# Kernel tuning notes

Hardware: AMD Instinct MI355X
Metric: run time of the kernel (lower is better)

Reference implementation:

```python
import jax, jax.numpy as jnp
import numpy as np

EMB = 1024
HEADS = 16
HEAD = EMB // HEADS
B, S = 4, 1024


def setup_inputs() -> dict:
    key = jax.random.key(0)
    ks = jax.random.split(key, 8)
    glorot = lambda k, shp: jax.random.normal(k, shp, jnp.float32) * np.sqrt(2.0 / (shp[-2] + shp[-1]))
    return {
        "inputs_for_keys": jax.random.normal(ks[0], (B, S, EMB), jnp.float32),
        "inputs_for_values": jax.random.normal(ks[1], (B, S, EMB), jnp.float32),
        "inputs_for_queries": jax.random.normal(ks[2], (B, S, EMB), jnp.float32),
        "Wk": glorot(ks[3], (HEADS, EMB, HEAD)),
        "Wv": glorot(ks[4], (HEADS, EMB, HEAD)),
        "Wq": glorot(ks[5], (HEADS, EMB, HEAD)),
        "Wo": glorot(ks[6], (EMB, EMB)),
        "bo": jnp.zeros((EMB,), jnp.float32),
    }


def reference(inputs_for_keys, inputs_for_values, inputs_for_queries, Wk, Wv, Wq, Wo, bo):
    # Batched equivalent of the per-head loop: project all heads at once.
    K = jnp.einsum("bse,hed->bhsd", inputs_for_keys, Wk)
    V = jnp.einsum("bse,hed->bhsd", inputs_for_values, Wv)
    Q = jnp.einsum("bse,hed->bhsd", inputs_for_queries, Wq)
    s_keys = K.shape[2]
    s_q = Q.shape[2]
    # causal mask: -inf strictly above diagonal (original: np.triu(ones*-inf, k=1))
    mask = jnp.where(jnp.triu(jnp.ones((s_q, s_keys), bool), k=1), -jnp.inf, 0.0).astype(jnp.float32)
    logits = jnp.einsum("bhqd,bhkd->bhqk", Q, K)
    # FAITHFUL quirk: original divides (logits + mask) by sqrt(window_size_keys)
    scores = jax.nn.softmax((logits + mask) / np.sqrt(s_keys), axis=-1)
    ctx = jnp.einsum("bhqk,bhkd->bhqd", scores, V)  # [B,H,Sq,Dh]
    # concat heads along last dim (head order matches loop order)
    concat = ctx.transpose(0, 2, 1, 3).reshape(ctx.shape[0], s_q, -1)  # [B,Sq,E]
    return jax.nn.relu(concat @ Wo + bo)
```

## Files before the change

### kernel.cpp

```cpp
#include <hip/hip_runtime.h>
#include <hip/hip_bf16.h>

typedef unsigned short u16;
typedef unsigned int   u32;
typedef __attribute__((ext_vector_type(4))) float f32x4;
typedef __attribute__((ext_vector_type(8))) short bf16x8;
typedef __attribute__((ext_vector_type(4))) short bf16x4;

#define EMB   1024
#define SEQ   1024
#define HEADS 16
#define DH    64
#define BATCH 4
#define BH    64
#define BS    4096
#define LDP   72
#define NEG_BIG (-1.0e30f)

__device__ __forceinline__ float b2f(u16 u){ return __uint_as_float(((u32)u) << 16); }
__device__ __forceinline__ u16 f2b(float f){
    u32 u = __float_as_uint(f);
    u32 r = u + 0x7fffu + ((u >> 16) & 1u);
    return (u16)(r >> 16);
}
__device__ __forceinline__ void zero4(f32x4& v){ v[0]=0.f; v[1]=0.f; v[2]=0.f; v[3]=0.f; }
__device__ __forceinline__ ushort4 pk4(float a, float b, float c, float d){
    ushort4 p; p.x = f2b(a); p.y = f2b(b); p.z = f2b(c); p.w = f2b(d); return p;
}

__device__ __forceinline__ void gld_lds16(const void* g, void* l){
    __builtin_amdgcn_global_load_lds(
        (const __attribute__((address_space(1))) u32*)g,
        (__attribute__((address_space(3))) u32*)l, 16, 0, 0);
}

__device__ __forceinline__ u16* tptr(u16* base, int row, int col ){
    const int phys = ((col >> 3) ^ (row & 7));
    return base + row * 64 + (phys << 3);
}
__device__ __forceinline__ const u16* tptrc(const u16* base, int row, int col ){
    const int phys = ((col >> 3) ^ (row & 7));
    return base + row * 64 + (phys << 3);
}
__device__ __forceinline__ const u16* tptr8c(const u16* base, int row, int col ){
    const int chunk = ((col >> 3) ^ (row & 7));
    return base + row * 64 + (chunk << 3) + (col & 7);
}

__device__ __forceinline__ void dot2_f32(const float* __restrict__ x,
                                         const float* __restrict__ w, const int ws,
                                         float& a0, float& a1)
{
    float s0 = 0.f, s1 = 0.f;
    for (int e = 0; e < EMB; e += 4) {
        const float4 xv = *(const float4*)(x + e);
        const float2 w0 = *(const float2*)(w + (size_t)(e + 0) * ws);
        const float2 w1 = *(const float2*)(w + (size_t)(e + 1) * ws);
        const float2 w2 = *(const float2*)(w + (size_t)(e + 2) * ws);
        const float2 w3 = *(const float2*)(w + (size_t)(e + 3) * ws);
        s0 += xv.x * w0.x; s1 += xv.x * w0.y;
        s0 += xv.y * w1.x; s1 += xv.y * w1.y;
        s0 += xv.z * w2.x; s1 += xv.z * w2.y;
        s0 += xv.w * w3.x; s1 += xv.w * w3.y;
    }
    a0 = s0; a1 = s1;
}


__global__ __launch_bounds__(256) void convert_x(
    const float* __restrict__ Xk, const float* __restrict__ Xv, const float* __restrict__ Xq,
    u16* __restrict__ XB)
{
    const int which = blockIdx.y;
    const float* __restrict__ src = (which == 0) ? Xk : (which == 1) ? Xv : Xq;
    const size_t off = (size_t)blockIdx.x * 1024 + threadIdx.x * 4;
    const float4 v = *(const float4*)(src + off);
    *(ushort4*)(XB + (size_t)which * 4194304 + off) = pk4(v.x, v.y, v.z, v.w);
}

__global__ __launch_bounds__(256) void transpose_w(
    const float* __restrict__ Wk, const float* __restrict__ Wv, const float* __restrict__ Wq,
    const float* __restrict__ Wo, u16* __restrict__ WT, u16* __restrict__ WoT)
{
    __shared__ u16 T[64][LDP];
    const int which = blockIdx.y;
    const int bx = blockIdx.x, t = threadIdx.x;

    if (which < 3) {
        const float* __restrict__ W = (which == 0) ? Wk : (which == 1) ? Wv : Wq;
        const int h = bx >> 4, e0 = (bx & 15) * 64;
        #pragma unroll
        for (int i = 0; i < 16; ++i) {
            const int idx = i * 256 + t;
            const int e = idx >> 6, d = idx & 63;
            T[d][e] = f2b(W[(size_t)h * (EMB * DH) + (size_t)(e0 + e) * DH + d]);
        }
        __syncthreads();
        u16* dstb = WT + (size_t)which * (EMB * EMB / 16) * 16;
        #pragma unroll
        for (int i = 0; i < 2; ++i) {
            const int idx = i * 256 + t;
            const int d = idx >> 3, e8 = (idx & 7) * 8;
            *(bf16x8*)(dstb + (size_t)(h * 64 + d) * EMB + e0 + e8) = *(const bf16x8*)&T[d][e8];
        }
    } else {
        const int j0 = (bx >> 4) * 64, e0 = (bx & 15) * 64;
        #pragma unroll
        for (int i = 0; i < 16; ++i) {
            const int idx = i * 256 + t;
            const int e = idx >> 6, d = idx & 63;
            T[d][e] = f2b(Wo[(size_t)(e0 + e) * EMB + j0 + d]);
        }
        __syncthreads();
        #pragma unroll
        for (int i = 0; i < 2; ++i) {
            const int idx = i * 256 + t;
            const int d = idx >> 3, e8 = (idx & 7) * 8;
            *(bf16x8*)(WoT + (size_t)(j0 + d) * EMB + e0 + e8) = *(const bf16x8*)&T[d][e8];
        }
    }
}

template<int MODE>
__global__ __launch_bounds__(256) void gemm128(
    const u16* __restrict__ XB, const u16* __restrict__ WT,
    u16* __restrict__ Qw, u16* __restrict__ Kw, u16* __restrict__ Vt,
    const float* __restrict__ bo, float* __restrict__ OUT)
{
    __shared__ u16 As[128 * 64];
    __shared__ u16 Bs[128 * 64];

    const int t = threadIdx.x;
    const int wave = t >> 6, lane = t & 63;
    const int quad = lane >> 4, l16 = lane & 15;
    const int wrow = wave >> 1, wcol = wave & 1;
    const int m0 = blockIdx.x * 128;
    const int n0 = blockIdx.y * 128;
    const int which = blockIdx.z;

    const u16* __restrict__ Ag = (MODE == 0) ? XB + (size_t)which * 4194304 : XB;
    const u16* __restrict__ Bg = (MODE == 0) ? WT + (size_t)which * 1048576 : WT;

    f32x4 acc[4][4];
    #pragma unroll
    for (int mi = 0; mi < 4; ++mi)
        #pragma unroll
        for (int ni = 0; ni < 4; ++ni) zero4(acc[mi][ni]);

    for (int k0 = 0; k0 < EMB; k0 += 64) {
        #pragma unroll
        for (int j = 0; j < 4; ++j) {
            const int cg = wave * 4 + j;
            const int c  = cg * 64 + lane;
            const int row = c >> 3;
            const int col = ((c ^ row) & 7) << 3;
            gld_lds16(Ag + (size_t)(m0 + row) * EMB + k0 + col, As + cg * 512);
            gld_lds16(Bg + (size_t)(n0 + row) * EMB + k0 + col, Bs + cg * 512);
        }
        __syncthreads();

        #pragma unroll
        for (int kb = 0; kb < 2; ++kb) {
            bf16x8 af[4], bf[4];
            #pragma unroll
            for (int mi = 0; mi < 4; ++mi)
                af[mi] = *(const bf16x8*)tptr(As, wrow * 64 + mi * 16 + l16, kb * 32 + quad * 8);
            #pragma unroll
            for (int ni = 0; ni < 4; ++ni)
                bf[ni] = *(const bf16x8*)tptr(Bs, wcol * 64 + ni * 16 + l16, kb * 32 + quad * 8);
            #pragma unroll
            for (int mi = 0; mi < 4; ++mi)
                #pragma unroll
                for (int ni = 0; ni < 4; ++ni)
                    acc[mi][ni] = __builtin_amdgcn_mfma_f32_16x16x32_bf16(af[mi], bf[ni], acc[mi][ni], 0, 0, 0);
        }
        __syncthreads();
    }

    #pragma unroll
    for (int mi = 0; mi < 4; ++mi) {
        const int r = m0 + wrow * 64 + mi * 16 + quad * 4;
        #pragma unroll
        for (int ni = 0; ni < 4; ++ni) {
            const int j = n0 + wcol * 64 + ni * 16 + l16;
            if (MODE == 1) {
                const float bias = bo[j];
                #pragma unroll
                for (int reg = 0; reg < 4; ++reg) {
                    float v = acc[mi][ni][reg] + bias;
                    if (v < 0.f) v = 0.f;
                    OUT[(size_t)(r + reg) * EMB + j] = v;
                }
            } else {
                const int h = j >> 6, d = j & 63;
                const int b = r >> 10, s = r & (SEQ - 1);
                const int bh = b * HEADS + h;
                if (which == 1) {
                    *(ushort4*)(Vt + ((size_t)bh * DH + d) * SEQ + s) =
                        pk4(acc[mi][ni][0], acc[mi][ni][1], acc[mi][ni][2], acc[mi][ni][3]);
                } else {
                    u16* dst = (which == 0) ? Kw : Qw;
                    const float qsc = (which == 2) ? 0.03125f : 1.0f;
                    #pragma unroll
                    for (int reg = 0; reg < 4; ++reg)
                        dst[((size_t)bh * SEQ + s + reg) * DH + d] = f2b(acc[mi][ni][reg] * qsc);
                }
            }
        }
    }
}

__global__ __launch_bounds__(256) void attn_flash2(
    const u16* __restrict__ Qg, const u16* __restrict__ Kg, const u16* __restrict__ Vg,
    u16* __restrict__ CTXb)
{
    __shared__ u16 Ks[2][64 * 64];
    __shared__ u16 Vs[2][64 * 64];

    const int t = threadIdx.x;
    const int wave = t >> 6, lane = t & 63;
    const int quad = lane >> 4, l16 = lane & 15;
    const int bh = blockIdx.y;
    const int qt = (blockIdx.x + (blockIdx.y >> 2)) & 15;
    const int b = bh >> 4, h = bh & (HEADS - 1);
    const int q0 = qt * 64;

    const u16* __restrict__ Kbase = Kg + (size_t)bh * SEQ * DH;
    const u16* __restrict__ Vbase = Vg + (size_t)bh * DH * SEQ;

    bf16x8 qf[2];
    {
        const u16* qrow = Qg + ((size_t)bh * SEQ + q0 + wave * 16 + l16) * DH;
        qf[0] = *(const bf16x8*)(qrow + quad * 8);
        qf[1] = *(const bf16x8*)(qrow + 32 + quad * 8);
    }

    #pragma unroll
    for (int i = 0; i < 2; ++i) {
        const int c = i * 256 + t;
        const int row = c >> 3, col8 = (c & 7) * 8;
        const bf16x8 kv = *(const bf16x8*)(Kbase + (size_t)row * DH + col8);
        const bf16x8 vv = *(const bf16x8*)(Vbase + (size_t)row * SEQ + col8);
        *(bf16x8*)tptr(&Ks[0][0], row, col8) = kv;
        *(bf16x8*)tptr(&Vs[0][0], row, col8) = vv;
    }

    float m = NEG_BIG, l = 0.f;
    f32x4 oacc[4];
    #pragma unroll
    for (int nd = 0; nd < 4; ++nd) zero4(oacc[nd]);

    __syncthreads();

    const int qin = wave * 16 + l16;
    int cur = 0;
    for (int c = 0; c <= qt; ++c) {
        const int kn = ((c < qt) ? c + 1 : qt) * 64;
        bf16x8 kpre[2], vpre[2];
        #pragma unroll
        for (int i = 0; i < 2; ++i) {
            const int cc = i * 256 + t;
            const int row = cc >> 3, col8 = (cc & 7) * 8;
            kpre[i] = *(const bf16x8*)(Kbase + (size_t)(kn + row) * DH + col8);
            vpre[i] = *(const bf16x8*)(Vbase + (size_t)row * SEQ + kn + col8);
        }

        const u16* Kc = &Ks[cur][0];
        const u16* Vc = &Vs[cur][0];

        f32x4 sacc[4];
        #pragma unroll
        for (int ni = 0; ni < 4; ++ni) zero4(sacc[ni]);
        __builtin_amdgcn_s_setprio(1);
        #pragma unroll
        for (int kb = 0; kb < 2; ++kb) {
            #pragma unroll
            for (int ni = 0; ni < 4; ++ni) {
                const bf16x8 kf = *(const bf16x8*)tptrc(Kc, ni * 16 + l16, kb * 32 + quad * 8);
                sacc[ni] = __builtin_amdgcn_mfma_f32_16x16x32_bf16(kf, qf[kb], sacc[ni], 0, 0, 0);
            }
        }
        __builtin_amdgcn_s_setprio(0);

        const bool diag = (c == qt);
        float mx = m;
        #pragma unroll
        for (int ni = 0; ni < 4; ++ni) {
            #pragma unroll
            for (int reg = 0; reg < 4; ++reg) {
                float s = sacc[ni][reg];
                if (diag && (ni * 16 + quad * 4 + reg > qin)) s = NEG_BIG;
                sacc[ni][reg] = s;
                mx = fmaxf(mx, s);
            }
        }
        mx = fmaxf(mx, __shfl_xor(mx, 16));
        mx = fmaxf(mx, __shfl_xor(mx, 32));
        const float alpha = __expf(m - mx);
        m = mx;
        float rs = 0.f;
        bf16x4 pa[4];
        #pragma unroll
        for (int ni = 0; ni < 4; ++ni) {
            const float p0 = __expf(sacc[ni][0] - mx);
            const float p1 = __expf(sacc[ni][1] - mx);
            const float p2 = __expf(sacc[ni][2] - mx);
            const float p3 = __expf(sacc[ni][3] - mx);
            rs += (p0 + p1) + (p2 + p3);
            bf16x4 pk;
            pk[0] = (short)f2b(p0); pk[1] = (short)f2b(p1);
            pk[2] = (short)f2b(p2); pk[3] = (short)f2b(p3);
            pa[ni] = pk;
        }
        rs += __shfl_xor(rs, 16);
        rs += __shfl_xor(rs, 32);
        l = l * alpha + rs;

        #pragma unroll
        for (int reg = 0; reg < 4; ++reg) {
            const float ar = __shfl(alpha, quad * 4 + reg);
            #pragma unroll
            for (int nd = 0; nd < 4; ++nd) oacc[nd][reg] *= ar;
        }

        __builtin_amdgcn_s_setprio(1);
        #pragma unroll
        for (int ks = 0; ks < 4; ++ks) {
            #pragma unroll
            for (int nd = 0; nd < 4; ++nd) {
                const bf16x4 vf = *(const bf16x4*)tptr8c(Vc, nd * 16 + l16, ks * 16 + quad * 4);
                oacc[nd] = __builtin_amdgcn_mfma_f32_16x16x16bf16_1k(pa[ks], vf, oacc[nd], 0, 0, 0);
            }
        }
        __builtin_amdgcn_s_setprio(0);

        const int nxt = cur ^ 1;
        #pragma unroll
        for (int i = 0; i < 2; ++i) {
            const int cc = i * 256 + t;
            const int row = cc >> 3, col8 = (cc & 7) * 8;
            *(bf16x8*)tptr(&Ks[nxt][0], row, col8) = kpre[i];
            *(bf16x8*)tptr(&Vs[nxt][0], row, col8) = vpre[i];
        }
        __syncthreads();
        cur = nxt;
    }

    #pragma unroll
    for (int reg = 0; reg < 4; ++reg) {
        const float il = 1.f / __shfl(l, quad * 4 + reg);
        const int q = q0 + wave * 16 + quad * 4 + reg;
        #pragma unroll
        for (int nd = 0; nd < 4; ++nd) {
            const int d = nd * 16 + l16;
            CTXb[(size_t)(b * SEQ + q) * EMB + h * DH + d] = f2b(oacc[nd][reg] * il);
        }
    }
}


__global__ __launch_bounds__(256) void qkv_proj_mfma(
    const float* __restrict__ Xk, const float* __restrict__ Xv, const float* __restrict__ Xq,
    const float* __restrict__ Wk, const float* __restrict__ Wv, const float* __restrict__ Wq,
    u16* __restrict__ Kw, u16* __restrict__ Vw, u16* __restrict__ Qw)
{
    __shared__ u16 As[128][LDP];
    __shared__ u16 Bs[64][LDP];

    const int which = blockIdx.z;
    const float* __restrict__ X = (which == 0) ? Xk : (which == 1) ? Xv : Xq;
    const float* __restrict__ W = (which == 0) ? Wk : (which == 1) ? Wv : Wq;

    const int h    = blockIdx.y;
    const int m0   = blockIdx.x * 128;
    const int t    = threadIdx.x;
    const int wave = t >> 6, lane = t & 63;
    const int quad = lane >> 4, l16 = lane & 15;

    f32x4 acc[2][4];
    #pragma unroll
    for (int mi = 0; mi < 2; ++mi)
        #pragma unroll
        for (int ni = 0; ni < 4; ++ni) zero4(acc[mi][ni]);

    const size_t wbase = (size_t)h * EMB * DH;
    for (int k0 = 0; k0 < EMB; k0 += 64) {
        #pragma unroll
        for (int i = 0; i < 8; ++i) {
            const int idx = i * 256 + t;
            const int r = idx >> 4, c4 = (idx & 15) * 4;
            const float4 v = *(const float4*)(X + (size_t)(m0 + r) * EMB + k0 + c4);
            *(ushort4*)&As[r][c4] = pk4(v.x, v.y, v.z, v.w);
        }
        #pragma unroll
        for (int i = 0; i < 4; ++i) {
            const int d  = t & 63;
            const int e0 = (t >> 6) * 4 + i * 16;
            const float v0 = W[wbase + (size_t)(k0 + e0 + 0) * DH + d];
            const float v1 = W[wbase + (size_t)(k0 + e0 + 1) * DH + d];
            const float v2 = W[wbase + (size_t)(k0 + e0 + 2) * DH + d];
            const float v3 = W[wbase + (size_t)(k0 + e0 + 3) * DH + d];
            *(ushort4*)&Bs[d][e0] = pk4(v0, v1, v2, v3);
        }
        __syncthreads();

        #pragma unroll
        for (int kb = 0; kb < 2; ++kb) {
            bf16x8 bfr[4];
            #pragma unroll
            for (int ni = 0; ni < 4; ++ni)
                bfr[ni] = *(const bf16x8*)&Bs[ni * 16 + l16][kb * 32 + quad * 8];
            #pragma unroll
            for (int mi = 0; mi < 2; ++mi) {
                const bf16x8 af = *(const bf16x8*)&As[wave * 32 + mi * 16 + l16][kb * 32 + quad * 8];
                #pragma unroll
                for (int ni = 0; ni < 4; ++ni)
                    acc[mi][ni] = __builtin_amdgcn_mfma_f32_16x16x32_bf16(af, bfr[ni], acc[mi][ni], 0, 0, 0);
            }
        }
        __syncthreads();
    }

    const int b  = m0 >> 10;
    const int bh = b * HEADS + h;
    u16* __restrict__ RowDst = (which == 0) ? Kw : Qw;
    #pragma unroll
    for (int mi = 0; mi < 2; ++mi) {
        const int s_base = (m0 & (SEQ - 1)) + wave * 32 + mi * 16 + quad * 4;
        #pragma unroll
        for (int ni = 0; ni < 4; ++ni) {
            const int d = ni * 16 + l16;
            if (which != 1) {
                #pragma unroll
                for (int reg = 0; reg < 4; ++reg)
                    RowDst[((size_t)bh * SEQ + s_base + reg) * DH + d] = f2b(acc[mi][ni][reg]);
            } else {
                *(ushort4*)(Vw + ((size_t)bh * DH + d) * SEQ + s_base) =
                    pk4(acc[mi][ni][0], acc[mi][ni][1], acc[mi][ni][2], acc[mi][ni][3]);
            }
        }
    }
}

template<bool QWS, bool TOWS>
__global__ __launch_bounds__(256) void attn_flash(
    const float* __restrict__ Xq, const float* __restrict__ Wq,
    const u16* __restrict__ Qg, const u16* __restrict__ Kg, const u16* __restrict__ Vg,
    u16* __restrict__ CTXb, float* __restrict__ CTXf)
{
    __shared__ u16 Qs[64][LDP];
    union KVU {
        struct { u16 Ks[64][LDP]; u16 Vt[64][LDP]; } kv;
        struct { u16 Xs[64][LDP]; u16 WT[64][LDP]; } pr;
    };
    __shared__ KVU uu;
    __shared__ u16 Ps[64][LDP];

    const int t    = threadIdx.x;
    const int wave = t >> 6, lane = t & 63;
    const int quad = lane >> 4, l16 = lane & 15;
    const int qt = blockIdx.x, bh = blockIdx.y;
    const int b  = bh >> 4, h = bh & (HEADS - 1);
    const int q0 = qt * 64;

    if (QWS) {
        #pragma unroll
        for (int i = 0; i < 4; ++i) {
            const int idx = i * 256 + t;
            const int r = idx >> 4, c4 = (idx & 15) * 4;
            *(ushort4*)&Qs[r][c4] = *(const ushort4*)(Qg + ((size_t)bh * SEQ + q0 + r) * DH + c4);
        }
    } else {
        f32x4 qacc[4];
        #pragma unroll
        for (int ni = 0; ni < 4; ++ni) zero4(qacc[ni]);
        const size_t wbase = (size_t)h * EMB * DH;
        for (int k0 = 0; k0 < EMB; k0 += 64) {
            #pragma unroll
            for (int i = 0; i < 4; ++i) {
                const int idx = i * 256 + t;
                const int r = idx >> 4, c4 = (idx & 15) * 4;
                const float4 v = *(const float4*)(Xq + (size_t)(b * SEQ + q0 + r) * EMB + k0 + c4);
                *(ushort4*)&uu.pr.Xs[r][c4] = pk4(v.x, v.y, v.z, v.w);
            }
            #pragma unroll
            for (int i = 0; i < 4; ++i) {
                const int d  = t & 63;
                const int e0 = (t >> 6) * 4 + i * 16;
                const float v0 = Wq[wbase + (size_t)(k0 + e0 + 0) * DH + d];
                const float v1 = Wq[wbase + (size_t)(k0 + e0 + 1) * DH + d];
                const float v2 = Wq[wbase + (size_t)(k0 + e0 + 2) * DH + d];
                const float v3 = Wq[wbase + (size_t)(k0 + e0 + 3) * DH + d];
                *(ushort4*)&uu.pr.WT[d][e0] = pk4(v0, v1, v2, v3);
            }
            __syncthreads();
            #pragma unroll
            for (int kb = 0; kb < 2; ++kb) {
                const bf16x8 af = *(const bf16x8*)&uu.pr.Xs[wave * 16 + l16][kb * 32 + quad * 8];
                #pragma unroll
                for (int ni = 0; ni < 4; ++ni) {
                    const bf16x8 bf = *(const bf16x8*)&uu.pr.WT[ni * 16 + l16][kb * 32 + quad * 8];
                    qacc[ni] = __builtin_amdgcn_mfma_f32_16x16x32_bf16(af, bf, qacc[ni], 0, 0, 0);
                }
            }
            __syncthreads();
        }
        #pragma unroll
        for (int ni = 0; ni < 4; ++ni)
            #pragma unroll
            for (int reg = 0; reg < 4; ++reg)
                Qs[wave * 16 + quad * 4 + reg][ni * 16 + l16] = f2b(qacc[ni][reg]);
    }

    float m[4], l[4];
    #pragma unroll
    for (int reg = 0; reg < 4; ++reg) { m[reg] = NEG_BIG; l[reg] = 0.f; }
    f32x4 oacc[4];
    #pragma unroll
    for (int ni = 0; ni < 4; ++ni) zero4(oacc[ni]);
    __syncthreads();

    for (int c = 0; c <= qt; ++c) {
        const int k0 = c * 64;

        #pragma unroll
        for (int i = 0; i < 4; ++i) {
            const int idx = i * 256 + t;
            const int r = idx >> 4, c4 = (idx & 15) * 4;
            *(ushort4*)&uu.kv.Ks[r][c4] = *(const ushort4*)(Kg + ((size_t)bh * SEQ + k0 + r) * DH + c4);
        }
        #pragma unroll
        for (int i = 0; i < 4; ++i) {
            const int idx = i * 256 + t;
            const int r = idx >> 4, c4 = (idx & 15) * 4;
            *(ushort4*)&uu.kv.Vt[r][c4] = *(const ushort4*)(Vg + ((size_t)bh * DH + r) * SEQ + k0 + c4);
        }
        __syncthreads();

        f32x4 sacc[4];
        #pragma unroll
        for (int ni = 0; ni < 4; ++ni) zero4(sacc[ni]);
        #pragma unroll
        for (int kb = 0; kb < 2; ++kb) {
            const bf16x8 af = *(const bf16x8*)&Qs[wave * 16 + l16][kb * 32 + quad * 8];
            #pragma unroll
            for (int ni = 0; ni < 4; ++ni) {
                const bf16x8 bf = *(const bf16x8*)&uu.kv.Ks[ni * 16 + l16][kb * 32 + quad * 8];
                sacc[ni] = __builtin_amdgcn_mfma_f32_16x16x32_bf16(af, bf, sacc[ni], 0, 0, 0);
            }
        }

        const bool diag = (c == qt);
        #pragma unroll
        for (int reg = 0; reg < 4; ++reg) {
            const int rloc = quad * 4 + reg;
            float sv[4];
            #pragma unroll
            for (int ni = 0; ni < 4; ++ni) {
                float s = sacc[ni][reg] * 0.03125f;
                if (diag && (ni * 16 + l16 > wave * 16 + rloc)) s = NEG_BIG;
                sv[ni] = s;
            }
            float mx = fmaxf(fmaxf(sv[0], sv[1]), fmaxf(sv[2], sv[3]));
            mx = fmaxf(mx, m[reg]);
            #pragma unroll
            for (int off = 1; off < 16; off <<= 1) mx = fmaxf(mx, __shfl_xor(mx, off));
            const float alpha = __expf(m[reg] - mx);
            float rs = 0.f;
            #pragma unroll
            for (int ni = 0; ni < 4; ++ni) {
                const float p = __expf(sv[ni] - mx);
                Ps[wave * 16 + rloc][ni * 16 + l16] = f2b(p);
                rs += p;
            }
            #pragma unroll
            for (int off = 1; off < 16; off <<= 1) rs += __shfl_xor(rs, off);
            l[reg] = l[reg] * alpha + rs;
            m[reg] = mx;
            #pragma unroll
            for (int ni = 0; ni < 4; ++ni) oacc[ni][reg] *= alpha;
        }
        __syncthreads();

        #pragma unroll
        for (int kb = 0; kb < 2; ++kb) {
            const bf16x8 af = *(const bf16x8*)&Ps[wave * 16 + l16][kb * 32 + quad * 8];
            #pragma unroll
            for (int ni = 0; ni < 4; ++ni) {
                const bf16x8 bf = *(const bf16x8*)&uu.kv.Vt[ni * 16 + l16][kb * 32 + quad * 8];
                oacc[ni] = __builtin_amdgcn_mfma_f32_16x16x32_bf16(af, bf, oacc[ni], 0, 0, 0);
            }
        }
        __syncthreads();
    }

    float il[4];
    #pragma unroll
    for (int reg = 0; reg < 4; ++reg) il[reg] = 1.f / l[reg];
    #pragma unroll
    for (int ni = 0; ni < 4; ++ni) {
        const int d = ni * 16 + l16;
        #pragma unroll
        for (int reg = 0; reg < 4; ++reg) {
            const int q = wave * 16 + quad * 4 + reg;
            const float val = oacc[ni][reg] * il[reg];
            const size_t off = ((size_t)(b * SEQ + q0 + q)) * EMB + h * DH + d;
            if (TOWS) CTXb[off] = f2b(val);
            else      CTXf[off] = val;
        }
    }
}

__global__ __launch_bounds__(256) void out_proj_mfma(
    const u16* __restrict__ CTXb, const float* __restrict__ Wo,
    const float* __restrict__ bo, float* __restrict__ OUT)
{
    __shared__ u16 As[128][LDP];
    __shared__ u16 Bs[64][LDP];

    const int m0 = blockIdx.x * 128;
    const int n0 = blockIdx.y * 64;
    const int t = threadIdx.x;
    const int wave = t >> 6, lane = t & 63;
    const int quad = lane >> 4, l16 = lane & 15;

    f32x4 acc[2][4];
    #pragma unroll
    for (int mi = 0; mi < 2; ++mi)
        #pragma unroll
        for (int ni = 0; ni < 4; ++ni) zero4(acc[mi][ni]);

    for (int k0 = 0; k0 < EMB; k0 += 64) {
        #pragma unroll
        for (int i = 0; i < 8; ++i) {
            const int idx = i * 256 + t;
            const int r = idx >> 4, c4 = (idx & 15) * 4;
            *(ushort4*)&As[r][c4] = *(const ushort4*)(CTXb + (size_t)(m0 + r) * EMB + k0 + c4);
        }
        #pragma unroll
        for (int i = 0; i < 4; ++i) {
            const int d  = t & 63;
            const int e0 = (t >> 6) * 4 + i * 16;
            const float v0 = Wo[(size_t)(k0 + e0 + 0) * EMB + n0 + d];
            const float v1 = Wo[(size_t)(k0 + e0 + 1) * EMB + n0 + d];
            const float v2 = Wo[(size_t)(k0 + e0 + 2) * EMB + n0 + d];
            const float v3 = Wo[(size_t)(k0 + e0 + 3) * EMB + n0 + d];
            *(ushort4*)&Bs[d][e0] = pk4(v0, v1, v2, v3);
        }
        __syncthreads();
        #pragma unroll
        for (int kb = 0; kb < 2; ++kb) {
            bf16x8 bfr[4];
            #pragma unroll
            for (int ni = 0; ni < 4; ++ni)
                bfr[ni] = *(const bf16x8*)&Bs[ni * 16 + l16][kb * 32 + quad * 8];
            #pragma unroll
            for (int mi = 0; mi < 2; ++mi) {
                const bf16x8 af = *(const bf16x8*)&As[wave * 32 + mi * 16 + l16][kb * 32 + quad * 8];
                #pragma unroll
                for (int ni = 0; ni < 4; ++ni)
                    acc[mi][ni] = __builtin_amdgcn_mfma_f32_16x16x32_bf16(af, bfr[ni], acc[mi][ni], 0, 0, 0);
            }
        }
        __syncthreads();
    }

    #pragma unroll
    for (int mi = 0; mi < 2; ++mi) {
        const int row = m0 + wave * 32 + mi * 16 + quad * 4;
        #pragma unroll
        for (int ni = 0; ni < 4; ++ni) {
            const int col = n0 + ni * 16 + l16;
            const float bias = bo[col];
            #pragma unroll
            for (int reg = 0; reg < 4; ++reg) {
                float v = acc[mi][ni][reg] + bias;
                if (v < 0.f) v = 0.f;
                OUT[(size_t)(row + reg) * EMB + col] = v;
            }
        }
    }
}

__global__ __launch_bounds__(256) void out_proj_inplace(
    float* __restrict__ OUT, const float* __restrict__ Wo, const float* __restrict__ bo)
{
    __shared__ float Xs[8][EMB];
    const int t    = threadIdx.x;
    const int row0 = blockIdx.x * 8;
    {
        const float4* src = (const float4*)(OUT + (size_t)row0 * EMB);
        float4* dst = (float4*)&Xs[0][0];
        #pragma unroll
        for (int i = 0; i < 8; ++i) dst[i * 256 + t] = src[i * 256 + t];
    }
    __syncthreads();
    const int r  = t >> 5;
    const int j0 = (t & 31) * 2;
    const float* xrow = Xs[r];
    for (int jb = 0; jb < 16; ++jb) {
        const int j = jb * 64 + j0;
        float a0, a1;
        dot2_f32(xrow, Wo + j, EMB, a0, a1);
        a0 += bo[j];     if (a0 < 0.f) a0 = 0.f;
        a1 += bo[j + 1]; if (a1 < 0.f) a1 = 0.f;
        float* op = OUT + (size_t)(row0 + r) * EMB + j;
        op[0] = a0; op[1] = a1;
    }
}

extern "C" void kernel_launch(void* const* d_in, const int* in_sizes, int n_in,
                              void* d_out, int out_size, void* d_ws, size_t ws_size,
                              hipStream_t stream)
{
    const float* Xk = (const float*)d_in[0];
    const float* Xv = (const float*)d_in[1];
    const float* Xq = (const float*)d_in[2];
    const float* Wk = (const float*)d_in[3];
    const float* Wv = (const float*)d_in[4];
    const float* Wq = (const float*)d_in[5];
    const float* Wo = (const float*)d_in[6];
    const float* bo = (const float*)d_in[7];
    float* OUT = (float*)d_out;
    (void)in_sizes; (void)n_in; (void)out_size;

    const size_t SEGE = (size_t)BH * SEQ * DH;
    const size_t SEGB = SEGE * sizeof(u16);

    const size_t XB_OFF  = 0;
    const size_t WT_OFF  = 3 * SEGE;
    const size_t WOT_OFF = WT_OFF + 3 * (EMB * EMB / 64) * 64;
    const size_t QW_OFF  = WOT_OFF + (size_t)EMB * EMB;
    const size_t KW_OFF  = QW_OFF + SEGE;
    const size_t VT_OFF  = KW_OFF + SEGE;
    const size_t TIER_A_BYTES = (VT_OFF + SEGE) * sizeof(u16);

    if (ws_size >= TIER_A_BYTES) {
        u16* W16 = (u16*)d_ws;
        u16* XB  = W16 + XB_OFF;
        u16* WT  = W16 + WT_OFF;
        u16* WoT = W16 + WOT_OFF;
        u16* Qw  = W16 + QW_OFF;
        u16* Kw  = W16 + KW_OFF;
        u16* Vt  = W16 + VT_OFF;
        u16* CTX = XB;

        convert_x<<<dim3(4096, 3), 256, 0, stream>>>(Xk, Xv, Xq, XB);
        transpose_w<<<dim3(256, 4), 256, 0, stream>>>(Wk, Wv, Wq, Wo, WT, WoT);
        gemm128<0><<<dim3(32, 8, 3), 256, 0, stream>>>(XB, WT, Qw, Kw, Vt, nullptr, nullptr);
        attn_flash2<<<dim3(SEQ / 64, BH), 256, 0, stream>>>(Qw, Kw, Vt, CTX);
        gemm128<1><<<dim3(32, 8, 1), 256, 0, stream>>>(CTX, WoT, nullptr, nullptr, nullptr, bo, OUT);
    } else if (ws_size >= 4 * SEGB) {
        u16* Qw = (u16*)d_ws;
        u16* Kw = Qw + SEGE;
        u16* Vw = Kw + SEGE;
        u16* CT = Vw + SEGE;
        qkv_proj_mfma<<<dim3(32, HEADS, 3), 256, 0, stream>>>(Xk, Xv, Xq, Wk, Wv, Wq, Kw, Vw, Qw);
        attn_flash<true, true><<<dim3(SEQ / 64, BH), 256, 0, stream>>>(
            Xq, Wq, Qw, Kw, Vw, CT, nullptr);
        out_proj_mfma<<<dim3(32, EMB / 64), 256, 0, stream>>>(CT, Wo, bo, OUT);
    } else if (ws_size >= 3 * SEGB) {
        u16* Kw = (u16*)d_ws;
        u16* Vw = Kw + SEGE;
        u16* CT = Vw + SEGE;
        qkv_proj_mfma<<<dim3(32, HEADS, 2), 256, 0, stream>>>(Xk, Xv, Xq, Wk, Wv, Wq, Kw, Vw, nullptr);
        attn_flash<false, true><<<dim3(SEQ / 64, BH), 256, 0, stream>>>(
            Xq, Wq, nullptr, Kw, Vw, CT, nullptr);
        out_proj_mfma<<<dim3(32, EMB / 64), 256, 0, stream>>>(CT, Wo, bo, OUT);
    } else {
        u16* Kw = (u16*)d_ws;
        u16* Vw = Kw + SEGE;
        qkv_proj_mfma<<<dim3(32, HEADS, 2), 256, 0, stream>>>(Xk, Xv, Xq, Wk, Wv, Wq, Kw, Vw, nullptr);
        attn_flash<false, false><<<dim3(SEQ / 64, BH), 256, 0, stream>>>(
            Xq, Wq, nullptr, Kw, Vw, nullptr, OUT);
        out_proj_inplace<<<dim3(BS / 8), 256, 0, stream>>>(OUT, Wo, bo);
    }
}
```

Measured before the change: 212.3 us.

## Fuse fp32-to-bf16 input conversion into projection GEMM and double-buffer B tiles

Drops the separate convert_x kernel. The QKV projection GEMM now loads the fp32 activations straight into registers, converts them to bf16 and writes them into LDS. The B (weight) tiles become double-buffered in LDS and are prefetched two k-steps ahead with direct global-to-LDS loads, with custom barriers to overlap loading and compute. This removes one launch and the write and re-read of the bf16 copy of the inputs. In exchange the GEMM reads twice as many activation bytes from fp32, uses more registers, and uses more LDS for the second B buffer.

Measured after the change: 219.5 us. +3.4%, slower.

```diff
diff --git a/kernel.cpp b/kernel.cpp
--- a/kernel.cpp
+++ b/kernel.cpp
@@ -67,17 +67,6 @@
 }
 
 
-__global__ __launch_bounds__(256) void convert_x(
-    const float* __restrict__ Xk, const float* __restrict__ Xv, const float* __restrict__ Xq,
-    u16* __restrict__ XB)
-{
-    const int which = blockIdx.y;
-    const float* __restrict__ src = (which == 0) ? Xk : (which == 1) ? Xv : Xq;
-    const size_t off = (size_t)blockIdx.x * 1024 + threadIdx.x * 4;
-    const float4 v = *(const float4*)(src + off);
-    *(ushort4*)(XB + (size_t)which * 4194304 + off) = pk4(v.x, v.y, v.z, v.w);
-}
-
 __global__ __launch_bounds__(256) void transpose_w(
     const float* __restrict__ Wk, const float* __restrict__ Wv, const float* __restrict__ Wq,
     const float* __restrict__ Wo, u16* __restrict__ WT, u16* __restrict__ WoT)
@@ -123,12 +112,13 @@
 
 template<int MODE>
 __global__ __launch_bounds__(256) void gemm128(
-    const u16* __restrict__ XB, const u16* __restrict__ WT,
+    const float* __restrict__ X0, const float* __restrict__ X1, const float* __restrict__ X2,
+    const u16* __restrict__ Ab, const u16* __restrict__ WT,
     u16* __restrict__ Qw, u16* __restrict__ Kw, u16* __restrict__ Vt,
     const float* __restrict__ bo, float* __restrict__ OUT)
 {
     __shared__ u16 As[128 * 64];
-    __shared__ u16 Bs[128 * 64];
+    __shared__ u16 Bs[2][128 * 64];
 
     const int t = threadIdx.x;
     const int wave = t >> 6, lane = t & 63;
@@ -138,7 +128,8 @@
     const int n0 = blockIdx.y * 128;
     const int which = blockIdx.z;
 
-    const u16* __restrict__ Ag = (MODE == 0) ? XB + (size_t)which * 4194304 : XB;
+    const float* __restrict__ Xa = (MODE == 0)
+        ? ((which == 0) ? X0 : (which == 1) ? X1 : X2) : (const float*)nullptr;
     const u16* __restrict__ Bg = (MODE == 0) ? WT + (size_t)which * 1048576 : WT;
 
     f32x4 acc[4][4];
@@ -147,34 +138,91 @@
         #pragma unroll
         for (int ni = 0; ni < 4; ++ni) zero4(acc[mi][ni]);
 
-    for (int k0 = 0; k0 < EMB; k0 += 64) {
+    float4 araw[8];
+    bf16x8 abf[4];
+
+    auto LOAD_A = [&](int kk){
+        #pragma unroll
+        for (int i = 0; i < 4; ++i) {
+            const int c = i * 256 + t;
+            const int row = c >> 3, col8 = (c & 7) * 8;
+            if constexpr (MODE == 0) {
+                const float* s = Xa + (size_t)(m0 + row) * EMB + kk + col8;
+                araw[i * 2]     = *(const float4*)s;
+                araw[i * 2 + 1] = *(const float4*)(s + 4);
+            } else {
+                abf[i] = *(const bf16x8*)(Ab + (size_t)(m0 + row) * EMB + kk + col8);
+            }
+        }
+    };
+    auto COMMIT_A = [&](){
+        #pragma unroll
+        for (int i = 0; i < 4; ++i) {
+            const int c = i * 256 + t;
+            const int row = c >> 3, col8 = (c & 7) * 8;
+            if constexpr (MODE == 0) {
+                union { bf16x8 v; ushort4 u[2]; } pk;
+                const float4 v0 = araw[i * 2], v1 = araw[i * 2 + 1];
+                pk.u[0] = pk4(v0.x, v0.y, v0.z, v0.w);
+                pk.u[1] = pk4(v1.x, v1.y, v1.z, v1.w);
+                *(bf16x8*)tptr(As, row, col8) = pk.v;
+            } else {
+                *(bf16x8*)tptr(As, row, col8) = abf[i];
+            }
+        }
+    };
+    auto STAGE_B = [&](int kk, int buf){
         #pragma unroll
         for (int j = 0; j < 4; ++j) {
             const int cg = wave * 4 + j;
             const int c  = cg * 64 + lane;
             const int row = c >> 3;
             const int col = ((c ^ row) & 7) << 3;
-            gld_lds16(Ag + (size_t)(m0 + row) * EMB + k0 + col, As + cg * 512);
-            gld_lds16(Bg + (size_t)(n0 + row) * EMB + k0 + col, Bs + cg * 512);
-        }
-        __syncthreads();
-
+            gld_lds16(Bg + (size_t)(n0 + row) * EMB + kk + col, &Bs[buf][cg * 512]);
+        }
+    };
+    auto COMPUTE = [&](const u16* Bc){
         #pragma unroll
         for (int kb = 0; kb < 2; ++kb) {
             bf16x8 af[4], bf[4];
             #pragma unroll
             for (int mi = 0; mi < 4; ++mi)
-                af[mi] = *(const bf16x8*)tptr(As, wrow * 64 + mi * 16 + l16, kb * 32 + quad * 8);
+                af[mi] = *(const bf16x8*)tptrc(As, wrow * 64 + mi * 16 + l16, kb * 32 + quad * 8);
             #pragma unroll
             for (int ni = 0; ni < 4; ++ni)
-                bf[ni] = *(const bf16x8*)tptr(Bs, wcol * 64 + ni * 16 + l16, kb * 32 + quad * 8);
+                bf[ni] = *(const bf16x8*)tptrc(Bc, wcol * 64 + ni * 16 + l16, kb * 32 + quad * 8);
             #pragma unroll
             for (int mi = 0; mi < 4; ++mi)
                 #pragma unroll
                 for (int ni = 0; ni < 4; ++ni)
                     acc[mi][ni] = __builtin_amdgcn_mfma_f32_16x16x32_bf16(af[mi], bf[ni], acc[mi][ni], 0, 0, 0);
         }
-        __syncthreads();
+    };
+    auto BAR = [&](){
+        __builtin_amdgcn_sched_barrier(0);
+        asm volatile("s_waitcnt lgkmcnt(0)" ::: "memory");
+        __builtin_amdgcn_s_barrier();
+        __builtin_amdgcn_sched_barrier(0);
+    };
+
+    LOAD_A(0);
+    STAGE_B(0, 0);
+    STAGE_B(64, 1);
+    COMMIT_A();
+    __syncthreads();
+    COMPUTE(&Bs[0][0]);
+    BAR();
+    LOAD_A(64);
+    STAGE_B(128, 0);
+
+    for (int k = 1; k < 16; ++k) {
+        const int k0 = k * 64;
+        COMMIT_A();
+        BAR();
+        COMPUTE(&Bs[k & 1][0]);
+        BAR();
+        if (k < 15) LOAD_A(k0 + 64);
+        if (k < 14) STAGE_B(k0 + 128, k & 1);
     }
 
     #pragma unroll
@@ -737,19 +785,19 @@
 
     if (ws_size >= TIER_A_BYTES) {
         u16* W16 = (u16*)d_ws;
-        u16* XB  = W16 + XB_OFF;
         u16* WT  = W16 + WT_OFF;
         u16* WoT = W16 + WOT_OFF;
         u16* Qw  = W16 + QW_OFF;
         u16* Kw  = W16 + KW_OFF;
         u16* Vt  = W16 + VT_OFF;
-        u16* CTX = XB;
-
-        convert_x<<<dim3(4096, 3), 256, 0, stream>>>(Xk, Xv, Xq, XB);
+        u16* CTX = W16 + XB_OFF;
+
         transpose_w<<<dim3(256, 4), 256, 0, stream>>>(Wk, Wv, Wq, Wo, WT, WoT);
-        gemm128<0><<<dim3(32, 8, 3), 256, 0, stream>>>(XB, WT, Qw, Kw, Vt, nullptr, nullptr);
+        gemm128<0><<<dim3(32, 8, 3), 256, 0, stream>>>(
+            Xk, Xv, Xq, nullptr, WT, Qw, Kw, Vt, nullptr, nullptr);
         attn_flash2<<<dim3(SEQ / 64, BH), 256, 0, stream>>>(Qw, Kw, Vt, CTX);
-        gemm128<1><<<dim3(32, 8, 1), 256, 0, stream>>>(CTX, WoT, nullptr, nullptr, nullptr, bo, OUT);
+        gemm128<1><<<dim3(32, 8, 1), 256, 0, stream>>>(
+            nullptr, nullptr, nullptr, CTX, WoT, nullptr, nullptr, nullptr, bo, OUT);
     } else if (ws_size >= 4 * SEGB) {
         u16* Qw = (u16*)d_ws;
         u16* Kw = Qw + SEGE;
```
